# Optimization experiments

Hardware: AMD Instinct MI355X
Metric: run time of the kernel (lower is better)

## Reference

```python
import jax, jax.numpy as jnp
import numpy as np

B, N, D, K = 8, 2048, 256, 8192


def setup_inputs() -> dict:
    key = jax.random.key(0)
    k1, k2 = jax.random.split(key)
    x = jax.random.normal(k1, (B, N, D), dtype=jnp.float32)          # encoder output z_e (identity encoder)
    codebook = jax.random.normal(k2, (K, D), dtype=jnp.float32)      # nn.Parameter(codebook_size, codebook_dim)
    return {"x": x, "codebook": codebook}


def reference(x, codebook):
    z_e = x  # identity encoder
    # Squared Euclidean distances via matmul expansion: ||z||^2 - 2 z.c^T + ||c||^2 -> (B, N, K)
    z2 = jnp.sum(z_e * z_e, axis=-1, keepdims=True)                   # (B, N, 1)
    c2 = jnp.sum(codebook * codebook, axis=-1)                        # (K,)
    cross = jnp.einsum('bnd,kd->bnk', z_e, codebook)                  # (B, N, K)
    distances = z2 - 2.0 * cross + c2                                 # (B, N, K)
    indices = jnp.argmin(distances, axis=-1)                          # (B, N) int
    z_q = codebook[indices]                                           # gather -> (B, N, D)
    x_recon = z_q  # identity decoder
    return (x_recon, z_e, z_q, indices)
```

## Files before the change

kernel.cpp:

```cpp
#include <hip/hip_runtime.h>
#include <stdint.h>


#define M_ROWS 16384
#define D_DIM  256
#define K_CB   8192
#define NSPLIT 16
#define CHUNK  64
#define EPS 20.0f

typedef float f32x4 __attribute__((ext_vector_type(4)));
typedef int   int4v __attribute__((ext_vector_type(4)));
typedef int   int8v __attribute__((ext_vector_type(8)));

__device__ __forceinline__ uint32_t umin32(uint32_t a, uint32_t b) { return a < b ? a : b; }
__device__ __forceinline__ uint32_t umax32(uint32_t a, uint32_t b) { return a > b ? a : b; }

__device__ __forceinline__ uint32_t fmin32(uint32_t a, uint32_t b) {
  return __float_as_uint(fminf(__uint_as_float(a), __uint_as_float(b)));
}
__device__ __forceinline__ uint32_t fmed32(uint32_t a, uint32_t b, uint32_t c) {
  return __float_as_uint(__builtin_amdgcn_fmed3f(
      __uint_as_float(a), __uint_as_float(b), __uint_as_float(c)));
}

__device__ __forceinline__ void gld_lds16(const void* g, void* l) {
  __builtin_amdgcn_global_load_lds((__attribute__((address_space(1))) void*)g,
                                   (__attribute__((address_space(3))) void*)l,
                                   16, 0, 0);
}

__device__ __forceinline__ float rtne3(float f) {
  uint32_t u = __float_as_uint(f);
  u = (u + 0x0007FFFFu + ((u >> 20) & 1u)) & 0xFFF00000u;
  return __uint_as_float(u);
}

__device__ __forceinline__ uint32_t fp8x4(const f32x4 v) {
  int p = __builtin_amdgcn_cvt_pk_fp8_f32(rtne3(v[0]), rtne3(v[1]), 0, false);
  p = __builtin_amdgcn_cvt_pk_fp8_f32(rtne3(v[2]), rtne3(v[3]), p, true);
  return (uint32_t)p;
}

__global__ __launch_bounds__(256) void prep(const float* __restrict__ x,
                                            const float* __restrict__ cb,
                                            uint8_t* __restrict__ Ap,
                                            uint8_t* __restrict__ Bp,
                                            float* __restrict__ c2s,
                                            float* __restrict__ out_ze) {
  const int w = threadIdx.x >> 6, lane = threadIdx.x & 63;
  if (blockIdx.x < M_ROWS / 4) {
    const int row = blockIdx.x * 4 + w;
    const f32x4 v = *(const f32x4*)(x + (size_t)row * D_DIM + lane * 4);
    f32x4 nv;
#pragma unroll
    for (int t = 0; t < 4; ++t) nv[t] = -2.0f * v[t];
    *(uint32_t*)(Ap + (size_t)row * D_DIM + lane * 4) = fp8x4(nv);
    *(f32x4*)(out_ze + (size_t)row * D_DIM + lane * 4) = v;
  } else {
    const int row = (blockIdx.x - M_ROWS / 4) * 4 + w;
    const f32x4 v = *(const f32x4*)(cb + (size_t)row * D_DIM + lane * 4);
    *(uint32_t*)(Bp + (size_t)row * D_DIM + lane * 4) = fp8x4(v);
    double s = 0.0;
#pragma unroll
    for (int t = 0; t < 4; ++t) s += (double)v[t] * (double)v[t];
#pragma unroll
    for (int m = 1; m < 64; m <<= 1) s += __shfl_xor(s, m, 64);
    if (lane == 0) c2s[row] = (float)s + 1024.0f;
  }
}

__global__ __launch_bounds__(256, 3) void vq_main(const uint8_t* __restrict__ Ap,
                                                  const uint8_t* __restrict__ Bp,
                                                  const float* __restrict__ c2s,
                                                  uint4* __restrict__ part) {
  __shared__ uint8_t Bs[2][CHUNK * D_DIM];

  const int w    = threadIdx.x >> 6;
  const int lane = threadIdx.x & 63;
  const int fr   = lane & 15;
  const int fq   = lane >> 4;

  const int rowBase = blockIdx.x * 128 + w * 32;
  const int colBase = blockIdx.y * 512;

  int8v af[2][2];
  {
    const uint8_t* ab = Ap + (size_t)(rowBase + fr) * D_DIM + fq * 32;
#pragma unroll
    for (int i = 0; i < 2; ++i)
#pragma unroll
      for (int kh = 0; kh < 2; ++kh)
        af[i][kh] = *(const int8v*)(ab + (size_t)(i * 16) * D_DIM + kh * 128);
  }

  const int dRow = lane >> 4;
  const int dChk = lane & 15;
  int goff[4];
#pragma unroll
  for (int ii = 0; ii < 4; ++ii) {
    const int rr = ii * 4 + dRow;
    goff[ii] = rr * D_DIM + ((dChk ^ rr) << 4);
  }

#define STAGE_DMA(c, buf)                                                      \
  {                                                                            \
    const uint8_t* gb = Bp + ((size_t)(colBase + (c) * CHUNK + w * 16) << 8);  \
    uint8_t* lb = &Bs[buf][w * 16 * D_DIM] + lane * 16;                        \
    _Pragma("unroll")                                                          \
    for (int ii = 0; ii < 4; ++ii)                                             \
      gld_lds16(gb + goff[ii], lb + ii * 4 * D_DIM);                           \
  }

  uint32_t t1[2][4], t2[2][4], t3[2][4], t4[2][4];
#pragma unroll
  for (int i = 0; i < 2; ++i)
#pragma unroll
    for (int r = 0; r < 4; ++r) {
      t1[i][r] = 0x7f7ffe00u; t2[i][r] = 0x7f7ffe00u;
      t3[i][r] = 0x7f7ffe00u; t4[i][r] = 0x7f7ffe00u;
    }

  const float* c2p = c2s + colBase + fr;
  const int y0 = (fq * 2) << 4;

  STAGE_DMA(0, 0);

  for (int c = 0; c < 512 / CHUNK; ++c) {
    __syncthreads();
    if (c < 512 / CHUNK - 1) STAGE_DMA(c + 1, (c + 1) & 1);

    const uint8_t* bsb = Bs[c & 1];
    const int cb0 = c * CHUNK;
    float cvv[4];
#pragma unroll
    for (int jj = 0; jj < 4; ++jj)
      cvv[jj] = c2p[cb0 + jj * 16];

#pragma unroll
    for (int jj = 0; jj < 4; ++jj) {
      const uint8_t* bp = bsb + (jj * 16 + fr) * D_DIM;
      const float cv = cvv[jj];
      f32x4 acc[2];
      acc[0] = (f32x4){cv, cv, cv, cv};
      acc[1] = (f32x4){cv, cv, cv, cv};
#pragma unroll
      for (int kh = 0; kh < 2; ++kh) {
        const int y = (y0 ^ (fr << 4)) ^ (kh << 7);
        const int4v lo = *(const int4v*)(bp + y);
        const int4v hi = *(const int4v*)(bp + (y ^ 16));
        int8v bf;
#pragma unroll
        for (int t = 0; t < 4; ++t) { bf[t] = lo[t]; bf[4 + t] = hi[t]; }
#pragma unroll
        for (int i = 0; i < 2; ++i)
          acc[i] = __builtin_amdgcn_mfma_scale_f32_16x16x128_f8f6f4(
              af[i][kh], bf, acc[i], 0, 0,
              0, 0x7f7f7f7f, 0, 0x7f7f7f7f);
      }
      const int col9 = cb0 + jj * 16 + fr;
#pragma unroll
      for (int i = 0; i < 2; ++i)
#pragma unroll
        for (int r = 0; r < 4; ++r) {
          const uint32_t p =
              (__float_as_uint(acc[i][r]) & ~511u) | (uint32_t)col9;
          const uint32_t o1 = t1[i][r], o2 = t2[i][r];
          const uint32_t o3 = t3[i][r], o4 = t4[i][r];
          t1[i][r] = fmin32(p, o1);
          t2[i][r] = fmed32(p, o1, o2);
          t3[i][r] = fmed32(p, o2, o3);
          t4[i][r] = fmed32(p, o3, o4);
        }
    }
  }

#pragma unroll
  for (int i = 0; i < 2; ++i)
#pragma unroll
    for (int r = 0; r < 4; ++r) {
      uint32_t a1 = t1[i][r], a2 = t2[i][r], a3 = t3[i][r], a4 = t4[i][r];
#pragma unroll
      for (int m = 1; m < 16; m <<= 1) {
        const uint32_t b1 = __shfl_xor(a1, m, 64);
        const uint32_t b2 = __shfl_xor(a2, m, 64);
        const uint32_t b3 = __shfl_xor(a3, m, 64);
        const uint32_t b4 = __shfl_xor(a4, m, 64);
        uint32_t c1 = umin32(a1, b4), c2_ = umin32(a2, b3);
        uint32_t c3 = umin32(a3, b2), c4 = umin32(a4, b1);
        uint32_t lo, hi;
        lo = umin32(c1, c3); hi = umax32(c1, c3); c1 = lo; c3 = hi;
        lo = umin32(c2_, c4); hi = umax32(c2_, c4); c2_ = lo; c4 = hi;
        lo = umin32(c1, c2_); hi = umax32(c1, c2_); c1 = lo; c2_ = hi;
        lo = umin32(c3, c4); hi = umax32(c3, c4); c3 = lo; c4 = hi;
        a1 = c1; a2 = c2_; a3 = c3; a4 = c4;
      }
      if (fr == 0) {
        const int row = rowBase + i * 16 + fq * 4 + r;
        part[(size_t)row * NSPLIT + blockIdx.y] = make_uint4(a1, a2, a3, a4);
      }
    }
}

__global__ __launch_bounds__(256) void vq_merge(const uint32_t* __restrict__ part,
                                                const float* __restrict__ x,
                                                const float* __restrict__ cb,
                                                float* __restrict__ out) {
  const int w = threadIdx.x >> 6, lane = threadIdx.x & 63;
  const int row = blockIdx.x * 4 + w;

  const uint32_t pk = part[(size_t)row * 64 + lane];
  const int gidx = (lane >> 2) * (K_CB / NSPLIT) + (int)(pk & 511u);

  uint32_t pmin = pk;
#pragma unroll
  for (int m = 1; m < 64; m <<= 1) {
    const uint32_t o = __shfl_xor(pmin, m, 64);
    pmin = pmin < o ? pmin : o;
  }
  const float vmin = __uint_as_float(pmin & ~511u);
  const float vme  = __uint_as_float(pk & ~511u);
  const unsigned long long mask = __ballot(vme <= vmin + EPS);
  const int nq = __popcll(mask);

  int winner;
  if (nq == 1) {
    winner = __shfl(gidx, __ffsll((long long)mask) - 1, 64);
  } else {
    const int g = lane >> 3, sub = lane & 7;
    const float* xrow = x + (size_t)row * D_DIM;
    double best = 1.0e300;
    int bidx = 0x7fffffff;
    unsigned long long bm = mask;
    for (int batch = 0; batch * 8 < nq; ++batch) {
      unsigned long long mm = bm;
#pragma unroll
      for (int t = 0; t < 7; ++t)
        if (t < g) mm &= mm - 1;
      const bool valid = (batch * 8 + g) < nq;
      const int qlane = valid ? (__ffsll((long long)mm) - 1) : 0;
      int ci = __shfl(gidx, qlane, 64);
      const float* cbp = cb + (size_t)ci * D_DIM;
      double s = 0.0;
#pragma unroll
      for (int t = 0; t < 8; ++t) {
        const int d = (t * 8 + sub) * 4;
        const f32x4 xv = *(const f32x4*)(xrow + d);
        const f32x4 cv = *(const f32x4*)(cbp + d);
#pragma unroll
        for (int u = 0; u < 4; ++u) {
          const double dx = (double)xv[u] - (double)cv[u];
          s += dx * dx;
        }
      }
#pragma unroll
      for (int m = 1; m < 8; m <<= 1) s += __shfl_xor(s, m, 64);
      if (!valid) { s = 1.0e300; ci = 0x7fffffff; }
      if (s < best || (s == best && ci < bidx)) { best = s; bidx = ci; }
#pragma unroll
      for (int t = 0; t < 8; ++t) bm &= bm - 1;
    }
#pragma unroll
    for (int m = 8; m < 64; m <<= 1) {
      const double ob = __shfl_xor(best, m, 64);
      const int oi = __shfl_xor(bidx, m, 64);
      if (ob < best || (ob == best && oi < bidx)) { best = ob; bidx = oi; }
    }
    winner = bidx;
  }

  float* out_recon = out;
  float* out_zq    = out + 2 * (size_t)M_ROWS * D_DIM;
  float* out_idx   = out + 3 * (size_t)M_ROWS * D_DIM;

  const f32x4 cv = *(const f32x4*)(cb + (size_t)winner * D_DIM + lane * 4);
  *(f32x4*)(out_recon + (size_t)row * D_DIM + lane * 4) = cv;
  *(f32x4*)(out_zq    + (size_t)row * D_DIM + lane * 4) = cv;
  if (lane == 0) out_idx[row] = (float)winner;
}

extern "C" void kernel_launch(void* const* d_in, const int* in_sizes, int n_in,
                              void* d_out, int out_size, void* d_ws, size_t ws_size,
                              hipStream_t stream) {
  const float* x  = (const float*)d_in[0];
  const float* cb = (const float*)d_in[1];
  float* out = (float*)d_out;

  char* ws = (char*)d_ws;
  float*    c2s  = (float*)ws;
  uint4*    part = (uint4*)(ws + 32768);
  uint8_t*  Ap   = (uint8_t*)(ws + 32768 + 4194304);
  uint8_t*  Bp   = Ap + (size_t)M_ROWS * D_DIM;
  if (ws_size < (size_t)(32768 + 4194304 + 4194304 + 2097152 + 4096)) return;

  float* out_ze = out + (size_t)M_ROWS * D_DIM;

  prep    <<<dim3(M_ROWS / 4 + K_CB / 4), dim3(256), 0, stream>>>(x, cb, Ap, Bp, c2s, out_ze);
  vq_main <<<dim3(M_ROWS / 128, NSPLIT), dim3(256), 0, stream>>>(Ap, Bp, c2s, part);
  vq_merge<<<dim3(M_ROWS / 4), dim3(256), 0, stream>>>((const uint32_t*)part, x, cb, out);
}
```

Baseline: 179.4 us.

## Load codebook fragments directly from global memory into registers, drop LDS staging

```diff
diff --git a/kernel.cpp b/kernel.cpp
--- a/kernel.cpp
+++ b/kernel.cpp
@@ -6,7 +6,6 @@
 #define D_DIM  256
 #define K_CB   8192
 #define NSPLIT 16
-#define CHUNK  64
 #define EPS 20.0f
 
 typedef float f32x4 __attribute__((ext_vector_type(4)));
@@ -22,12 +21,6 @@
 __device__ __forceinline__ uint32_t fmed32(uint32_t a, uint32_t b, uint32_t c) {
   return __float_as_uint(__builtin_amdgcn_fmed3f(
       __uint_as_float(a), __uint_as_float(b), __uint_as_float(c)));
-}
-
-__device__ __forceinline__ void gld_lds16(const void* g, void* l) {
-  __builtin_amdgcn_global_load_lds((__attribute__((address_space(1))) void*)g,
-                                   (__attribute__((address_space(3))) void*)l,
-                                   16, 0, 0);
 }
 
 __device__ __forceinline__ float rtne3(float f) {
@@ -70,12 +63,10 @@
   }
 }
 
-__global__ __launch_bounds__(256, 3) void vq_main(const uint8_t* __restrict__ Ap,
+__global__ __launch_bounds__(256, 4) void vq_main(const uint8_t* __restrict__ Ap,
                                                   const uint8_t* __restrict__ Bp,
                                                   const float* __restrict__ c2s,
                                                   uint4* __restrict__ part) {
-  __shared__ uint8_t Bs[2][CHUNK * D_DIM];
-
   const int w    = threadIdx.x >> 6;
   const int lane = threadIdx.x & 63;
   const int fr   = lane & 15;
@@ -94,24 +85,6 @@
         af[i][kh] = *(const int8v*)(ab + (size_t)(i * 16) * D_DIM + kh * 128);
   }
 
-  const int dRow = lane >> 4;
-  const int dChk = lane & 15;
-  int goff[4];
-#pragma unroll
-  for (int ii = 0; ii < 4; ++ii) {
-    const int rr = ii * 4 + dRow;
-    goff[ii] = rr * D_DIM + ((dChk ^ rr) << 4);
-  }
-
-#define STAGE_DMA(c, buf)                                                      \
-  {                                                                            \
-    const uint8_t* gb = Bp + ((size_t)(colBase + (c) * CHUNK + w * 16) << 8);  \
-    uint8_t* lb = &Bs[buf][w * 16 * D_DIM] + lane * 16;                        \
-    _Pragma("unroll")                                                          \
-    for (int ii = 0; ii < 4; ++ii)                                             \
-      gld_lds16(gb + goff[ii], lb + ii * 4 * D_DIM);                           \
-  }
-
   uint32_t t1[2][4], t2[2][4], t3[2][4], t4[2][4];
 #pragma unroll
   for (int i = 0; i < 2; ++i)
@@ -121,58 +94,54 @@
       t3[i][r] = 0x7f7ffe00u; t4[i][r] = 0x7f7ffe00u;
     }
 
-  const float* c2p = c2s + colBase + fr;
-  const int y0 = (fq * 2) << 4;
-
-  STAGE_DMA(0, 0);
-
-  for (int c = 0; c < 512 / CHUNK; ++c) {
-    __syncthreads();
-    if (c < 512 / CHUNK - 1) STAGE_DMA(c + 1, (c + 1) & 1);
-
-    const uint8_t* bsb = Bs[c & 1];
-    const int cb0 = c * CHUNK;
-    float cvv[4];
-#pragma unroll
-    for (int jj = 0; jj < 4; ++jj)
-      cvv[jj] = c2p[cb0 + jj * 16];
-
-#pragma unroll
-    for (int jj = 0; jj < 4; ++jj) {
-      const uint8_t* bp = bsb + (jj * 16 + fr) * D_DIM;
-      const float cv = cvv[jj];
-      f32x4 acc[2];
-      acc[0] = (f32x4){cv, cv, cv, cv};
-      acc[1] = (f32x4){cv, cv, cv, cv};
-#pragma unroll
-      for (int kh = 0; kh < 2; ++kh) {
-        const int y = (y0 ^ (fr << 4)) ^ (kh << 7);
-        const int4v lo = *(const int4v*)(bp + y);
-        const int4v hi = *(const int4v*)(bp + (y ^ 16));
-        int8v bf;
-#pragma unroll
-        for (int t = 0; t < 4; ++t) { bf[t] = lo[t]; bf[4 + t] = hi[t]; }
-#pragma unroll
-        for (int i = 0; i < 2; ++i)
-          acc[i] = __builtin_amdgcn_mfma_scale_f32_16x16x128_f8f6f4(
-              af[i][kh], bf, acc[i], 0, 0,
-              0, 0x7f7f7f7f, 0, 0x7f7f7f7f);
-      }
-      const int col9 = cb0 + jj * 16 + fr;
-#pragma unroll
-      for (int i = 0; i < 2; ++i)
-#pragma unroll
-        for (int r = 0; r < 4; ++r) {
-          const uint32_t p =
-              (__float_as_uint(acc[i][r]) & ~511u) | (uint32_t)col9;
-          const uint32_t o1 = t1[i][r], o2 = t2[i][r];
-          const uint32_t o3 = t3[i][r], o4 = t4[i][r];
-          t1[i][r] = fmin32(p, o1);
-          t2[i][r] = fmed32(p, o1, o2);
-          t3[i][r] = fmed32(p, o2, o3);
-          t4[i][r] = fmed32(p, o3, o4);
-        }
-    }
+  const uint8_t* bb = Bp + (size_t)(colBase + fr) * D_DIM + fq * 32;
+  const float*  c2p = c2s + colBase + fr;
+
+#define LOADB(dst, j)                                                          \
+  {                                                                            \
+    const uint8_t* gp_ = bb + (size_t)(j) * (16 * D_DIM);                      \
+    *(int4v*)&dst[0]       = *(const int4v*)(gp_);                             \
+    *((int4v*)&dst[0] + 1) = *(const int4v*)(gp_ + 16);                        \
+    *(int4v*)&dst[1]       = *(const int4v*)(gp_ + 128);                       \
+    *((int4v*)&dst[1] + 1) = *(const int4v*)(gp_ + 144);                       \
+  }
+
+#define COMPUTE(j, bfrag, cv)                                                  \
+  {                                                                            \
+    f32x4 acc[2];                                                              \
+    acc[0] = (f32x4){cv, cv, cv, cv};                \
+    acc[1] = (f32x4){cv, cv, cv, cv};                                          \
+    _Pragma("unroll")                                                          \
+    for (int i = 0; i < 2; ++i) {                                              \
+      acc[i] = __builtin_amdgcn_mfma_scale_f32_16x16x128_f8f6f4(               \
+          af[i][0], bfrag[0], acc[i], 0, 0, 0, 0x7f7f7f7f, 0, 0x7f7f7f7f);     \
+      acc[i] = __builtin_amdgcn_mfma_scale_f32_16x16x128_f8f6f4(               \
+          af[i][1], bfrag[1], acc[i], 0, 0, 0, 0x7f7f7f7f, 0, 0x7f7f7f7f);     \
+    }                                                                          \
+    const int col9 = (j) * 16 + fr;                                            \
+    _Pragma("unroll")                                                          \
+    for (int i = 0; i < 2; ++i)                                                \
+      _Pragma("unroll")                                                        \
+      for (int r = 0; r < 4; ++r) {                                            \
+        const uint32_t p =                                                     \
+            (__float_as_uint(acc[i][r]) & ~511u) | (uint32_t)col9;             \
+        const uint32_t o1 = t1[i][r], o2 = t2[i][r];                           \
+        const uint32_t o3 = t3[i][r], o4 = t4[i][r];                           \
+        t1[i][r] = fmin32(p, o1);                       \
+        t2[i][r] = fmed32(p, o1, o2);                                          \
+        t3[i][r] = fmed32(p, o2, o3);                                          \
+        t4[i][r] = fmed32(p, o3, o4);                                          \
+      }                                                                        \
+  }
+
+  int8v b0[2], b1[2];
+  float cv0, cv1;
+  LOADB(b0, 0); cv0 = c2p[0];
+  for (int jj = 0; jj < 32; jj += 2) {
+    LOADB(b1, jj + 1); cv1 = c2p[(jj + 1) * 16];
+    COMPUTE(jj, b0, cv0);
+    if (jj + 2 < 32) { LOADB(b0, jj + 2); cv0 = c2p[(jj + 2) * 16]; }
+    COMPUTE(jj + 1, b1, cv1);
   }
 
 #pragma unroll
@@ -182,12 +151,12 @@
       uint32_t a1 = t1[i][r], a2 = t2[i][r], a3 = t3[i][r], a4 = t4[i][r];
 #pragma unroll
       for (int m = 1; m < 16; m <<= 1) {
-        const uint32_t b1 = __shfl_xor(a1, m, 64);
-        const uint32_t b2 = __shfl_xor(a2, m, 64);
-        const uint32_t b3 = __shfl_xor(a3, m, 64);
-        const uint32_t b4 = __shfl_xor(a4, m, 64);
-        uint32_t c1 = umin32(a1, b4), c2_ = umin32(a2, b3);
-        uint32_t c3 = umin32(a3, b2), c4 = umin32(a4, b1);
+        const uint32_t b1_ = __shfl_xor(a1, m, 64);
+        const uint32_t b2_ = __shfl_xor(a2, m, 64);
+        const uint32_t b3_ = __shfl_xor(a3, m, 64);
+        const uint32_t b4_ = __shfl_xor(a4, m, 64);
+        uint32_t c1 = umin32(a1, b4_), c2_ = umin32(a2, b3_);
+        uint32_t c3 = umin32(a3, b2_), c4 = umin32(a4, b1_);
         uint32_t lo, hi;
         lo = umin32(c1, c3); hi = umax32(c1, c3); c1 = lo; c3 = hi;
         lo = umin32(c2_, c4); hi = umax32(c2_, c4); c2_ = lo; c4 = hi;
```

Measured after the change: 329.7 us. +83.8%, slower.
